# Kernel optimization log

Measured on AMD Instinct MI355X. Metric: run time of the kernel, lower is better.

The kernel has to match this reference:

```python
import jax, jax.numpy as jnp
import numpy as np

B, SWIN_D, VIT_D, E, H = 16384, 768, 512, 1024, 4
HD = E // H  # 256


def setup_inputs() -> dict:
    key = jax.random.key(0)
    ks = jax.random.split(key, 12)
    s = lambda fan_in: 1.0 / np.sqrt(fan_in)
    return {
        "swin_feat": jax.random.normal(ks[0], (B, SWIN_D), jnp.float32),
        "vit_feat": jax.random.normal(ks[1], (B, VIT_D), jnp.float32),
        # outer projections (nn.Linear: y = x @ W.T + b)
        "Wq": jax.random.uniform(ks[2], (E, SWIN_D), jnp.float32, -s(SWIN_D), s(SWIN_D)),
        "bq": jax.random.uniform(ks[3], (E,), jnp.float32, -s(SWIN_D), s(SWIN_D)),
        "Wk": jax.random.uniform(ks[4], (E, VIT_D), jnp.float32, -s(VIT_D), s(VIT_D)),
        "bk": jax.random.uniform(ks[5], (E,), jnp.float32, -s(VIT_D), s(VIT_D)),
        "Wv": jax.random.uniform(ks[6], (E, VIT_D), jnp.float32, -s(VIT_D), s(VIT_D)),
        "bv": jax.random.uniform(ks[7], (E,), jnp.float32, -s(VIT_D), s(VIT_D)),
        # nn.MultiheadAttention internal in_proj (stacked q,k,v) and out_proj
        "in_proj_w": jax.random.uniform(ks[8], (3 * E, E), jnp.float32, -s(E), s(E)),
        "in_proj_b": jnp.zeros((3 * E,), jnp.float32),
        "Wo": jax.random.uniform(ks[9], (E, E), jnp.float32, -s(E), s(E)),
        "bo": jnp.zeros((E,), jnp.float32),
    }


def reference(swin_feat, vit_feat, Wq, bq, Wk, bk, Wv, bv, in_proj_w, in_proj_b, Wo, bo):
    # outer projections -> [B, E] (seq_len = 1, so the seq dim is implicit)
    q = swin_feat @ Wq.T + bq
    k = vit_feat @ Wk.T + bk
    v = vit_feat @ Wv.T + bv
    # MultiheadAttention in-projection (split stacked weight)
    Wiq, Wik, Wiv = in_proj_w[:E], in_proj_w[E:2 * E], in_proj_w[2 * E:]
    biq, bik, biv = in_proj_b[:E], in_proj_b[E:2 * E], in_proj_b[2 * E:]
    q2 = (q @ Wiq.T + biq).reshape(B, H, HD)
    k2 = (k @ Wik.T + bik).reshape(B, H, HD)
    v2 = (v @ Wiv.T + biv).reshape(B, H, HD)
    # attention with q_len = kv_len = 1
    scale = 1.0 / np.sqrt(HD)
    scores = jnp.einsum('bhd,bhd->bh', q2, k2) * scale        # [B, H]
    w = jax.nn.softmax(scores[..., None], axis=-1)             # softmax over 1 key -> ones
    attn = w * v2                                              # [B, H, HD]
    out = attn.reshape(B, E) @ Wo.T + bo                       # out-projection
    return out
```

## Files before the change

kernel.cpp:

```cpp
#include <hip/hip_runtime.h>
#include <stdint.h>
#include <stddef.h>

#define E_DIM 1024

typedef __bf16 v8bf __attribute__((ext_vector_type(8)));
typedef float v4f __attribute__((ext_vector_type(4)));

__device__ __forceinline__ unsigned short f2bf(float x) {
  unsigned int u = __builtin_bit_cast(unsigned int, x);
  u += 0x7fffu + ((u >> 16) & 1u);
  return (unsigned short)(u >> 16);
}

template <int RB>
__device__ __forceinline__ int swz(int r, int c) {
  if constexpr (RB >= 128) return c ^ ((r & 7) << 4);
  else return c;
}

template <int ROWS, int BK, int F32>
__device__ __forceinline__ void stage(const char* __restrict__ G, int g0, int ldg,
                                      int k0, char* L, int tid) {
  constexpr int ESZ = F32 ? 4 : 2;
  constexpr int RB = BK * ESZ;
  constexpr int ITERS = (ROWS * RB) / 4096;
  const int wid = tid >> 6, lane = tid & 63;
#pragma unroll
  for (int it = 0; it < ITERS; ++it) {
    int lbase = it * 4096 + wid * 1024;
    int lin = lbase + lane * 16;
    int r = lin / RB, cb = lin % RB;
    int gcb = swz<RB>(r, cb);
    const char* g = G + ((size_t)(g0 + r) * ldg + k0) * ESZ + gcb;
    __builtin_amdgcn_global_load_lds((const __attribute__((address_space(1))) void*)g,
                                     (__attribute__((address_space(3))) void*)(L + lbase),
                                     16, 0, 0);
  }
}

template <int RB>
__device__ __forceinline__ v8bf fragA_f32(const char* L, int r, int kelem) {
  const char* p = L + r * RB;
  int o = swz<RB>(r, kelem * 4);
  float4 lo = *(const float4*)(p + o);
  float4 hi = *(const float4*)(p + (o ^ 16));
  v8bf f;
  f[0] = (__bf16)lo.x; f[1] = (__bf16)lo.y; f[2] = (__bf16)lo.z; f[3] = (__bf16)lo.w;
  f[4] = (__bf16)hi.x; f[5] = (__bf16)hi.y; f[6] = (__bf16)hi.z; f[7] = (__bf16)hi.w;
  return f;
}

template <int RB>
__device__ __forceinline__ v8bf frag_bf16(const char* L, int r, int kelem) {
  int o = swz<RB>(r, kelem * 2);
  return *(const v8bf*)(L + r * RB + o);
}

template <int BM, int BN, int BK, int FM, int FN, int AF32, int BF32>
__device__ __forceinline__ void compute_tile(const char* Al, const char* Bl,
                                             v4f (&acc)[FM][FN],
                                             int wr, int wc, int lr, int kg) {
  constexpr int RBA = BK * (AF32 ? 4 : 2);
  constexpr int RBB = BK * (BF32 ? 4 : 2);
  constexpr int TMW = BM / 2, TNW = BN / 2;
#pragma unroll
  for (int kk = 0; kk < BK / 32; ++kk) {
    const int ke = kk * 32 + kg * 8;
    v8bf a[FM], b[FN];
#pragma unroll
    for (int mi = 0; mi < FM; ++mi) {
      int ra = wr * TMW + mi * 16 + lr;
      if constexpr (AF32) a[mi] = fragA_f32<RBA>(Al, ra, ke);
      else                a[mi] = frag_bf16<RBA>(Al, ra, ke);
    }
#pragma unroll
    for (int ni = 0; ni < FN; ++ni) {
      int rb = wc * TNW + ni * 16 + lr;
      if constexpr (BF32) b[ni] = fragA_f32<RBB>(Bl, rb, ke);
      else                b[ni] = frag_bf16<RBB>(Bl, rb, ke);
    }
#pragma unroll
    for (int mi = 0; mi < FM; ++mi)
#pragma unroll
      for (int ni = 0; ni < FN; ++ni)
        acc[mi][ni] = __builtin_amdgcn_mfma_f32_16x16x32_bf16(a[mi], b[ni], acc[mi][ni], 0, 0, 0);
  }
}

__global__ __launch_bounds__(256) void prep1(const float* __restrict__ Wv,
                                             unsigned short* __restrict__ WvT,
                                             const float* __restrict__ Wiv,
                                             const float* __restrict__ bv,
                                             const float* __restrict__ biv,
                                             float* __restrict__ b1) {
  int bid = blockIdx.x;
  if (bid < 512) {
    __shared__ float tile[32][33];
    const int R = 1024, C = 512;
    int nbx = C >> 5;
    int bx = bid % nbx, by = bid / nbx;
    int tx = threadIdx.x & 31, ty = threadIdx.x >> 5;
#pragma unroll
    for (int i = 0; i < 32; i += 8)
      tile[ty + i][tx] = Wv[(size_t)(by * 32 + ty + i) * C + bx * 32 + tx];
    __syncthreads();
#pragma unroll
    for (int i = 0; i < 32; i += 8)
      WvT[(size_t)(bx * 32 + ty + i) * R + by * 32 + tx] = f2bf(tile[tx][ty + i]);
  } else {
    int r = (bid - 512) * 4 + (threadIdx.x >> 6);
    int lane = threadIdx.x & 63;
    float s = 0.f;
    for (int c = lane; c < 1024; c += 64) s += Wiv[(size_t)r * 1024 + c] * bv[c];
#pragma unroll
    for (int off = 32; off; off >>= 1) s += __shfl_down(s, off);
    if (lane == 0) b1[r] = s + biv[r];
  }
}

template <int BM, int BN, int BK, int FM, int FN, int OUTBF, int AF32, int BF32, int XCDSWZ>
__global__ __launch_bounds__(256) void gemm_bt(const void* __restrict__ Ag,
                                               const void* __restrict__ Bg,
                                               const float* __restrict__ bias,
                                               float* __restrict__ Cf,
                                               unsigned short* __restrict__ Cb,
                                               int M, int N, int K,
                                               const float* __restrict__ mvW,
                                               const float* __restrict__ mvx,
                                               const float* __restrict__ mvb,
                                               float* __restrict__ mvy) {
  constexpr int RBA = BK * (AF32 ? 4 : 2);
  constexpr int RBB = BK * (BF32 ? 4 : 2);
  __shared__ __align__(16) char Al0[BM * RBA];
  __shared__ __align__(16) char Al1[BM * RBA];
  __shared__ __align__(16) char Bl0[BN * RBB];
  __shared__ __align__(16) char Bl1[BN * RBB];
  const int nbn = N / BN;
  const int ngemm = nbn * (M / BM);
  int bid = blockIdx.x;
  const int tid = threadIdx.x;

  if (bid >= ngemm) {
    int r = (bid - ngemm) * 4 + (tid >> 6);
    int lane = tid & 63;
    float s = 0.f;
    for (int c = lane; c < 1024; c += 64) s += mvW[(size_t)r * 1024 + c] * mvx[c];
#pragma unroll
    for (int off = 32; off; off >>= 1) s += __shfl_down(s, off);
    if (lane == 0) mvy[r] = s + mvb[r];
    return;
  }

  int bm_i, bn_i;
  if (XCDSWZ) {
    int x = bid & 7, j = bid >> 3;
    bm_i = x + ((j >> 3) << 3);
    bn_i = j & 7;
  } else {
    bm_i = bid / nbn;
    bn_i = bid % nbn;
  }
  const int bm0 = bm_i * BM, bn0 = bn_i * BN;

  constexpr int TMW = BM / 2, TNW = BN / 2;
  const int lane = tid & 63;
  const int wid = tid >> 6;
  const int wr = wid >> 1, wc = wid & 1;
  const int lr = lane & 15;
  const int kg = lane >> 4;
  const char* Ac = (const char*)Ag;
  const char* Bc = (const char*)Bg;

  v4f acc[FM][FN];
#pragma unroll
  for (int i = 0; i < FM; ++i)
#pragma unroll
    for (int j = 0; j < FN; ++j) acc[i][j] = 0.f;

  const int NT = K / BK;
  stage<BM, BK, AF32>(Ac, bm0, K, 0, Al0, tid);
  stage<BN, BK, BF32>(Bc, bn0, K, 0, Bl0, tid);
  __syncthreads();

  for (int t = 0; t < NT; t += 2) {
    if (t + 1 < NT) {
      stage<BM, BK, AF32>(Ac, bm0, K, (t + 1) * BK, Al1, tid);
      stage<BN, BK, BF32>(Bc, bn0, K, (t + 1) * BK, Bl1, tid);
    }
    __builtin_amdgcn_sched_barrier(0);
    compute_tile<BM, BN, BK, FM, FN, AF32, BF32>(Al0, Bl0, acc, wr, wc, lr, kg);
    __syncthreads();

    if (t + 2 < NT) {
      stage<BM, BK, AF32>(Ac, bm0, K, (t + 2) * BK, Al0, tid);
      stage<BN, BK, BF32>(Bc, bn0, K, (t + 2) * BK, Bl0, tid);
    }
    __builtin_amdgcn_sched_barrier(0);
    compute_tile<BM, BN, BK, FM, FN, AF32, BF32>(Al1, Bl1, acc, wr, wc, lr, kg);
    __syncthreads();
  }

#pragma unroll
  for (int ni = 0; ni < FN; ++ni) {
    int col = bn0 + wc * TNW + ni * 16 + lr;
    float bz = bias ? bias[col] : 0.f;
#pragma unroll
    for (int mi = 0; mi < FM; ++mi) {
      int row0 = bm0 + wr * TMW + mi * 16 + kg * 4;
#pragma unroll
      for (int r = 0; r < 4; ++r) {
        float v = acc[mi][ni][r] + bz;
        if (OUTBF) Cb[(size_t)(row0 + r) * N + col] = f2bf(v);
        else       Cf[(size_t)(row0 + r) * N + col] = v;
      }
    }
  }
}

extern "C" void kernel_launch(void* const* d_in, const int* in_sizes, int n_in,
                              void* d_out, int out_size, void* d_ws, size_t ws_size,
                              hipStream_t stream) {
  const float* vit = (const float*)d_in[1];
  const float* Wv  = (const float*)d_in[6];
  const float* bv  = (const float*)d_in[7];
  const float* ipw = (const float*)d_in[8];
  const float* ipb = (const float*)d_in[9];
  const float* Wo  = (const float*)d_in[10];
  const float* bo  = (const float*)d_in[11];
  const float* Wiv = ipw + 2 * E_DIM * E_DIM;
  const float* biv = ipb + 2 * E_DIM;

  char* ws = (char*)d_ws;
  unsigned short* WvTb = (unsigned short*)(ws);
  unsigned short* Ttb  = (unsigned short*)(ws + (1 << 20));
  unsigned short* Wcb  = (unsigned short*)(ws + (2 << 20));
  float* b1 = (float*)(ws + (3 << 20));
  float* bc = (float*)(ws + (3 << 20) + 4096);

  prep1<<<768, 256, 0, stream>>>(Wv, WvTb, Wiv, bv, biv, b1);

  gemm_bt<64, 64, 64, 2, 2, 1, 0, 1, 0><<<128 + 256, 256, 0, stream>>>(
      WvTb, Wiv, nullptr, nullptr, Ttb, 512, 1024, 1024, Wo, b1, bo, bc);

  gemm_bt<64, 64, 64, 2, 2, 1, 1, 0, 0><<<128, 256, 0, stream>>>(
      Wo, Ttb, nullptr, nullptr, Wcb, 1024, 512, 1024,
      nullptr, nullptr, nullptr, nullptr);

  gemm_bt<128, 128, 32, 4, 4, 0, 1, 0, 1><<<1024, 256, 0, stream>>>(
      vit, Wcb, bc, (float*)d_out, nullptr, 16384, 1024, 512,
      nullptr, nullptr, nullptr, nullptr);
}
```

Baseline: 67.30 us.

## Stage fp32 GEMM operands through registers and store bf16 into shared memory

For fp32 operands, the kernel no longer copies fp32 tiles directly from global memory into LDS and converts them at fragment-read time. It now loads each next tile into registers with float4 loads, converts to bf16 after the current tile's MFMA compute, and writes bf16 into swizzled LDS. This halves LDS footprint and LDS read traffic for fp32 inputs and removes repeated conversion in the inner loop. The cost is more register pressure and a synchronous register-to-LDS write step, and the prefetch of tile t+1 now runs without checking t+1<NT.

```diff
diff --git a/kernel.cpp b/kernel.cpp
--- a/kernel.cpp
+++ b/kernel.cpp
@@ -19,11 +19,10 @@
   else return c;
 }
 
-template <int ROWS, int BK, int F32>
-__device__ __forceinline__ void stage(const char* __restrict__ G, int g0, int ldg,
-                                      int k0, char* L, int tid) {
-  constexpr int ESZ = F32 ? 4 : 2;
-  constexpr int RB = BK * ESZ;
+template <int ROWS, int BK>
+__device__ __forceinline__ void stageg(const char* __restrict__ G, int g0, int ldg,
+                                       int k0, char* L, int tid) {
+  constexpr int RB = BK * 2;
   constexpr int ITERS = (ROWS * RB) / 4096;
   const int wid = tid >> 6, lane = tid & 63;
 #pragma unroll
@@ -32,23 +31,37 @@
     int lin = lbase + lane * 16;
     int r = lin / RB, cb = lin % RB;
     int gcb = swz<RB>(r, cb);
-    const char* g = G + ((size_t)(g0 + r) * ldg + k0) * ESZ + gcb;
+    const char* g = G + ((size_t)(g0 + r) * ldg + k0) * 2 + gcb;
     __builtin_amdgcn_global_load_lds((const __attribute__((address_space(1))) void*)g,
                                      (__attribute__((address_space(3))) void*)(L + lbase),
                                      16, 0, 0);
   }
 }
 
-template <int RB>
-__device__ __forceinline__ v8bf fragA_f32(const char* L, int r, int kelem) {
-  const char* p = L + r * RB;
-  int o = swz<RB>(r, kelem * 4);
-  float4 lo = *(const float4*)(p + o);
-  float4 hi = *(const float4*)(p + (o ^ 16));
-  v8bf f;
-  f[0] = (__bf16)lo.x; f[1] = (__bf16)lo.y; f[2] = (__bf16)lo.z; f[3] = (__bf16)lo.w;
-  f[4] = (__bf16)hi.x; f[5] = (__bf16)hi.y; f[6] = (__bf16)hi.z; f[7] = (__bf16)hi.w;
-  return f;
+template <int ROWS, int BK>
+__device__ __forceinline__ void regload(const float* __restrict__ G, int g0, int ldg,
+                                        int k0, int tid, float4 (&r)[(ROWS * BK) / 1024]) {
+  constexpr int C4 = BK / 4;
+#pragma unroll
+  for (int p = 0; p < (ROWS * BK) / 1024; ++p) {
+    int i4 = p * 256 + tid;
+    int row = i4 / C4, c4 = i4 % C4;
+    r[p] = *reinterpret_cast<const float4*>(G + (size_t)(g0 + row) * ldg + k0 + c4 * 4);
+  }
+}
+
+template <int ROWS, int BK>
+__device__ __forceinline__ void cvtwrite(const float4 (&r)[(ROWS * BK) / 1024],
+                                         char* L, int tid) {
+  constexpr int C4 = BK / 4, RB = BK * 2;
+#pragma unroll
+  for (int p = 0; p < (ROWS * BK) / 1024; ++p) {
+    int i4 = p * 256 + tid;
+    int row = i4 / C4, c4 = i4 % C4;
+    ushort4 u;
+    u.x = f2bf(r[p].x); u.y = f2bf(r[p].y); u.z = f2bf(r[p].z); u.w = f2bf(r[p].w);
+    *reinterpret_cast<ushort4*>(L + row * RB + swz<RB>(row, c4 * 8)) = u;
+  }
 }
 
 template <int RB>
@@ -57,29 +70,22 @@
   return *(const v8bf*)(L + r * RB + o);
 }
 
-template <int BM, int BN, int BK, int FM, int FN, int AF32, int BF32>
+template <int BM, int BN, int BK, int FM, int FN>
 __device__ __forceinline__ void compute_tile(const char* Al, const char* Bl,
                                              v4f (&acc)[FM][FN],
                                              int wr, int wc, int lr, int kg) {
-  constexpr int RBA = BK * (AF32 ? 4 : 2);
-  constexpr int RBB = BK * (BF32 ? 4 : 2);
+  constexpr int RBA = BK * 2, RBB = BK * 2;
   constexpr int TMW = BM / 2, TNW = BN / 2;
 #pragma unroll
   for (int kk = 0; kk < BK / 32; ++kk) {
     const int ke = kk * 32 + kg * 8;
     v8bf a[FM], b[FN];
 #pragma unroll
-    for (int mi = 0; mi < FM; ++mi) {
-      int ra = wr * TMW + mi * 16 + lr;
-      if constexpr (AF32) a[mi] = fragA_f32<RBA>(Al, ra, ke);
-      else                a[mi] = frag_bf16<RBA>(Al, ra, ke);
-    }
-#pragma unroll
-    for (int ni = 0; ni < FN; ++ni) {
-      int rb = wc * TNW + ni * 16 + lr;
-      if constexpr (BF32) b[ni] = fragA_f32<RBB>(Bl, rb, ke);
-      else                b[ni] = frag_bf16<RBB>(Bl, rb, ke);
-    }
+    for (int mi = 0; mi < FM; ++mi)
+      a[mi] = frag_bf16<RBA>(Al, wr * TMW + mi * 16 + lr, ke);
+#pragma unroll
+    for (int ni = 0; ni < FN; ++ni)
+      b[ni] = frag_bf16<RBB>(Bl, wc * TNW + ni * 16 + lr, ke);
 #pragma unroll
     for (int mi = 0; mi < FM; ++mi)
 #pragma unroll
@@ -130,12 +136,10 @@
                                                const float* __restrict__ mvx,
                                                const float* __restrict__ mvb,
                                                float* __restrict__ mvy) {
-  constexpr int RBA = BK * (AF32 ? 4 : 2);
-  constexpr int RBB = BK * (BF32 ? 4 : 2);
-  __shared__ __align__(16) char Al0[BM * RBA];
-  __shared__ __align__(16) char Al1[BM * RBA];
-  __shared__ __align__(16) char Bl0[BN * RBB];
-  __shared__ __align__(16) char Bl1[BN * RBB];
+  __shared__ __align__(16) char Al0[BM * BK * 2];
+  __shared__ __align__(16) char Al1[BM * BK * 2];
+  __shared__ __align__(16) char Bl0[BN * BK * 2];
+  __shared__ __align__(16) char Bl1[BN * BK * 2];
   const int nbn = N / BN;
   const int ngemm = nbn * (M / BM);
   int bid = blockIdx.x;
@@ -171,6 +175,8 @@
   const int kg = lane >> 4;
   const char* Ac = (const char*)Ag;
   const char* Bc = (const char*)Bg;
+  const float* Af = (const float*)Ag;
+  const float* Bf = (const float*)Bg;
 
   v4f acc[FM][FN];
 #pragma unroll
@@ -178,26 +184,46 @@
 #pragma unroll
     for (int j = 0; j < FN; ++j) acc[i][j] = 0.f;
 
+  float4 ra[AF32 ? (BM * BK) / 1024 : 1];
+  float4 rb[BF32 ? (BN * BK) / 1024 : 1];
+
   const int NT = K / BK;
-  stage<BM, BK, AF32>(Ac, bm0, K, 0, Al0, tid);
-  stage<BN, BK, BF32>(Bc, bn0, K, 0, Bl0, tid);
+
+  if constexpr (AF32) regload<BM, BK>(Af, bm0, K, 0, tid, (float4(&)[(BM * BK) / 1024])ra);
+  else                stageg<BM, BK>(Ac, bm0, K, 0, Al0, tid);
+  if constexpr (BF32) regload<BN, BK>(Bf, bn0, K, 0, tid, (float4(&)[(BN * BK) / 1024])rb);
+  else                stageg<BN, BK>(Bc, bn0, K, 0, Bl0, tid);
+  if constexpr (AF32) cvtwrite<BM, BK>((float4(&)[(BM * BK) / 1024])ra, Al0, tid);
+  if constexpr (BF32) cvtwrite<BN, BK>((float4(&)[(BN * BK) / 1024])rb, Bl0, tid);
   __syncthreads();
 
   for (int t = 0; t < NT; t += 2) {
-    if (t + 1 < NT) {
-      stage<BM, BK, AF32>(Ac, bm0, K, (t + 1) * BK, Al1, tid);
-      stage<BN, BK, BF32>(Bc, bn0, K, (t + 1) * BK, Bl1, tid);
+    {
+      if constexpr (AF32) regload<BM, BK>(Af, bm0, K, (t + 1) * BK, tid, (float4(&)[(BM * BK) / 1024])ra);
+      else                stageg<BM, BK>(Ac, bm0, K, (t + 1) * BK, Al1, tid);
+      if constexpr (BF32) regload<BN, BK>(Bf, bn0, K, (t + 1) * BK, tid, (float4(&)[(BN * BK) / 1024])rb);
+      else                stageg<BN, BK>(Bc, bn0, K, (t + 1) * BK, Bl1, tid);
     }
     __builtin_amdgcn_sched_barrier(0);
-    compute_tile<BM, BN, BK, FM, FN, AF32, BF32>(Al0, Bl0, acc, wr, wc, lr, kg);
+    compute_tile<BM, BN, BK, FM, FN>(Al0, Bl0, acc, wr, wc, lr, kg);
+    {
+      if constexpr (AF32) cvtwrite<BM, BK>((float4(&)[(BM * BK) / 1024])ra, Al1, tid);
+      if constexpr (BF32) cvtwrite<BN, BK>((float4(&)[(BN * BK) / 1024])rb, Bl1, tid);
+    }
     __syncthreads();
 
     if (t + 2 < NT) {
-      stage<BM, BK, AF32>(Ac, bm0, K, (t + 2) * BK, Al0, tid);
-      stage<BN, BK, BF32>(Bc, bn0, K, (t + 2) * BK, Bl0, tid);
+      if constexpr (AF32) regload<BM, BK>(Af, bm0, K, (t + 2) * BK, tid, (float4(&)[(BM * BK) / 1024])ra);
+      else                stageg<BM, BK>(Ac, bm0, K, (t + 2) * BK, Al0, tid);
+      if constexpr (BF32) regload<BN, BK>(Bf, bn0, K, (t + 2) * BK, tid, (float4(&)[(BN * BK) / 1024])rb);
+      else                stageg<BN, BK>(Bc, bn0, K, (t + 2) * BK, Bl0, tid);
     }
     __builtin_amdgcn_sched_barrier(0);
-    compute_tile<BM, BN, BK, FM, FN, AF32, BF32>(Al1, Bl1, acc, wr, wc, lr, kg);
+    compute_tile<BM, BN, BK, FM, FN>(Al1, Bl1, acc, wr, wc, lr, kg);
+    if (t + 2 < NT) {
+      if constexpr (AF32) cvtwrite<BM, BK>((float4(&)[(BM * BK) / 1024])ra, Al0, tid);
+      if constexpr (BF32) cvtwrite<BN, BK>((float4(&)[(BN * BK) / 1024])rb, Bl0, tid);
+    }
     __syncthreads();
   }
 
```

New measurement: 72.53 us. 7.8% more time.
